# Kernel tuning notes

Hardware: AMD Instinct MI355X
Metric: run time of the kernel (lower is better)

## Reference

```python
import jax, jax.numpy as jnp
import numpy as np


def setup_inputs() -> dict:
    key = jax.random.key(0)
    ks = jax.random.split(key, 8)
    n_src, n_dst, n_edges = 100000, 50000, 600000
    d_in, d_out = 128, 128
    n_reuse, n_cache = 5000, 8000
    full_dst_len = n_dst + n_reuse

    feat_src = jax.random.normal(ks[0], (n_src, d_in), jnp.float32)
    src = jax.random.randint(ks[1], (n_edges,), 0, n_src)
    dst = jax.random.randint(ks[2], (n_edges,), 0, n_dst)
    # xavier-ish init for the two bias-free Linear layers (stored as [out, in] like torch)
    W_self = jax.random.normal(ks[3], (d_out, d_in), jnp.float32) / np.sqrt(d_in).astype(np.float32)
    W_neigh = jax.random.normal(ks[4], (d_out, d_in), jnp.float32) / np.sqrt(d_in).astype(np.float32)
    # reuse_indices must be unique positions within [0, full_dst_len)
    reuse_indices = jnp.sort(jax.random.permutation(ks[5], full_dst_len)[:n_reuse])
    reuse_embedding = jax.random.normal(ks[6], (n_reuse, d_out), jnp.float32)
    cache_indices = jax.random.randint(ks[7], (n_cache,), 0, full_dst_len)
    return dict(feat_src=feat_src, W_self=W_self, W_neigh=W_neigh,
                reuse_embedding=reuse_embedding, src=src, dst=dst,
                reuse_indices=reuse_indices, cache_indices=cache_indices,
                n_dst=n_dst)


def reference(feat_src, W_self, W_neigh, reuse_embedding, src, dst,
              reuse_indices, cache_indices, n_dst):
    # --- GraphSAGE 'mean' aggregation on a block graph ---
    feat_dst = feat_src[:n_dst]                         # [n_dst, D_in]
    msgs = feat_src[src]                                # [E, D_in] copy_src gather
    ssum = jax.ops.segment_sum(msgs, dst, num_segments=n_dst)          # [n_dst, D_in]
    deg = jax.ops.segment_sum(jnp.ones_like(msgs[:, 0]), dst, num_segments=n_dst)
    h_neigh = jnp.where(deg[:, None] > 0, ssum / jnp.maximum(deg, 1.0)[:, None], 0.0)
    rst = feat_dst @ W_self.T + h_neigh @ W_neigh.T     # fc_self + fc_neigh

    # --- cache-reuse scatter merge (flag == 0 path) ---
    n_reuse = reuse_indices.shape[0]
    full_dst_len = n_dst + n_reuse
    keep = jnp.ones((full_dst_len,), dtype=bool).at[reuse_indices].set(False)
    unprune_indices = jnp.nonzero(keep, size=n_dst)[0]  # np.delete equivalent
    full = jnp.zeros((full_dst_len, rst.shape[1]), rst.dtype)
    full = full.at[unprune_indices].set(rst).at[reuse_indices].set(reuse_embedding)
    cache_embedding = jax.lax.stop_gradient(full[cache_indices])  # .detach()
    return full, cache_embedding
```

## Files before the change

kernel.cpp:

```cpp
#include <hip/hip_runtime.h>

#define N_SRC   100000
#define N_DST   50000
#define D       128
#define MAXDEG  64

#define TOTAL_BLOCKS 2048
#define EDGE_BLOCKS  512

typedef __attribute__((ext_vector_type(8))) short bf16x8;
typedef __attribute__((ext_vector_type(4))) float f32x4;

__device__ __forceinline__ unsigned short f2bf(float f) {
    unsigned u = __float_as_uint(f);
    u += 0x7FFFu + ((u >> 16) & 1u);
    return (unsigned short)(u >> 16);
}
__device__ __forceinline__ float bf2f(unsigned short u) {
    return __uint_as_float((unsigned)u << 16);
}

__global__ __launch_bounds__(256)
void prep_build_kernel(const int* __restrict__ src,
                       const int* __restrict__ dst,
                       int* __restrict__ ell,
                       int* __restrict__ cnt,
                       int n_edges,
                       const int* __restrict__ reuse_idx,
                       int* __restrict__ rowpos, int n_reuse,
                       const float* __restrict__ Wself,
                       const float* __restrict__ Wneigh,
                       unsigned short* __restrict__ wbf,
                       const float* __restrict__ feat,
                       unsigned int* __restrict__ featbf_u32) {
    if (blockIdx.x < EDGE_BLOCKS) {
        int eid = blockIdx.x * 256 + threadIdx.x;
        const int estride = EDGE_BLOCKS * 256;
        for (int e0 = eid; e0 < n_edges; e0 += 4 * estride) {
            int e1 = e0 + estride, e2 = e0 + 2 * estride, e3 = e0 + 3 * estride;
            bool v1 = e1 < n_edges, v2 = e2 < n_edges, v3 = e3 < n_edges;
            int d0 = dst[e0], s0 = src[e0];
            int d1 = 0, s1 = 0, d2 = 0, s2 = 0, d3 = 0, s3 = 0;
            if (v1) { d1 = dst[e1]; s1 = src[e1]; }
            if (v2) { d2 = dst[e2]; s2 = src[e2]; }
            if (v3) { d3 = dst[e3]; s3 = src[e3]; }
            int p0 = atomicAdd(&cnt[d0], 1);
            int p1 = v1 ? atomicAdd(&cnt[d1], 1) : MAXDEG;
            int p2 = v2 ? atomicAdd(&cnt[d2], 1) : MAXDEG;
            int p3 = v3 ? atomicAdd(&cnt[d3], 1) : MAXDEG;
            if (p0 < MAXDEG) ell[(size_t)d0 * MAXDEG + p0] = s0;
            if (p1 < MAXDEG) ell[(size_t)d1 * MAXDEG + p1] = s1;
            if (p2 < MAXDEG) ell[(size_t)d2 * MAXDEG + p2] = s2;
            if (p3 < MAXDEG) ell[(size_t)d3 * MAXDEG + p3] = s3;
        }
    } else {
        int stid = (blockIdx.x - EDGE_BLOCKS) * 256 + threadIdx.x;
        const int sstride = (TOTAL_BLOCKS - EDGE_BLOCKS) * 256;

        if (stid < N_DST) {
            int lo = 0, hi = n_reuse;
            while (lo < hi) {
                int mid = (lo + hi) >> 1;
                if (reuse_idx[mid] - mid > stid) hi = mid; else lo = mid + 1;
            }
            rowpos[stid] = stid + lo;
        }

        if (stid < 128 * 256) {
            int n = stid >> 8;
            int k = stid & 255;
            float v = (k < 128) ? Wself[n * 128 + k] : Wneigh[n * 128 + (k - 128)];
            wbf[stid] = f2bf(v);
        }

        const int n4 = N_SRC * (D / 4);
        for (int i = stid; i < n4; i += sstride) {
            float4 v = *(const float4*)(feat + (size_t)i * 4);
            uint2 o;
            o.x = (unsigned)f2bf(v.x) | ((unsigned)f2bf(v.y) << 16);
            o.y = (unsigned)f2bf(v.z) | ((unsigned)f2bf(v.w) << 16);
            *(uint2*)(featbf_u32 + (size_t)i * 2) = o;
        }
    }
}

__global__ __launch_bounds__(256)
void gather_bf16_kernel(const unsigned short* __restrict__ featbf,
                        const int* __restrict__ ell,
                        const int* __restrict__ cnt,
                        uint4* __restrict__ hneigh_u4) {
    int gid  = blockIdx.x * blockDim.x + threadIdx.x;
    int row  = gid >> 4;
    int lane = gid & 15;
    if (row >= N_DST) return;

    int deg = cnt[row];
    int n = min(deg, MAXDEG);
    float inv = 1.0f / fmaxf((float)deg, 1.0f);
    const int* rell = ell + (size_t)row * MAXDEG;

    float acc[8];
#pragma unroll
    for (int k = 0; k < 8; ++k) acc[k] = 0.f;

    union U { uint4 v; unsigned short us[8]; };
    int j = 0;
    for (; j + 4 <= n; j += 4) {
        int s0 = rell[j + 0];
        int s1 = rell[j + 1];
        int s2 = rell[j + 2];
        int s3 = rell[j + 3];
        U a, b, c, d;
        a.v = *(const uint4*)(featbf + (size_t)s0 * D + lane * 8);
        b.v = *(const uint4*)(featbf + (size_t)s1 * D + lane * 8);
        c.v = *(const uint4*)(featbf + (size_t)s2 * D + lane * 8);
        d.v = *(const uint4*)(featbf + (size_t)s3 * D + lane * 8);
#pragma unroll
        for (int k = 0; k < 8; ++k)
            acc[k] += (bf2f(a.us[k]) + bf2f(b.us[k])) + (bf2f(c.us[k]) + bf2f(d.us[k]));
    }
    for (; j < n; ++j) {
        int s = rell[j];
        U a;
        a.v = *(const uint4*)(featbf + (size_t)s * D + lane * 8);
#pragma unroll
        for (int k = 0; k < 8; ++k) acc[k] += bf2f(a.us[k]);
    }
    uint4 o;
    o.x = (unsigned)f2bf(acc[0] * inv) | ((unsigned)f2bf(acc[1] * inv) << 16);
    o.y = (unsigned)f2bf(acc[2] * inv) | ((unsigned)f2bf(acc[3] * inv) << 16);
    o.z = (unsigned)f2bf(acc[4] * inv) | ((unsigned)f2bf(acc[5] * inv) << 16);
    o.w = (unsigned)f2bf(acc[6] * inv) | ((unsigned)f2bf(acc[7] * inv) << 16);
    hneigh_u4[(size_t)row * 16 + lane] = o;
}

__global__ __launch_bounds__(256, 2)
void gemm_kernel(const unsigned short* __restrict__ featbf,
                 const unsigned short* __restrict__ hneigh,
                 const unsigned short* __restrict__ wbf,
                 const int* __restrict__ rowpos,
                 float* __restrict__ full) {
    __shared__ unsigned short Wl[128 * 256];

    int tid = threadIdx.x;
    {
        int n = tid >> 1;
        int ckbase = (tid & 1) * 16;
        const uint4* s = (const uint4*)(wbf + n * 256);
        uint4* d = (uint4*)(Wl + n * 256);
#pragma unroll
        for (int i = 0; i < 16; ++i) {
            int ck = ckbase + i;
            d[ck ^ (n & 7)] = s[ck];
        }
    }
    __syncthreads();

    int wv   = tid >> 6;
    int lane = tid & 63;
    int l15  = lane & 15;
    int q    = lane >> 4;
    int rowbase = blockIdx.x * 128 + wv * 32;

    f32x4 acc[2][8];
#pragma unroll
    for (int rt = 0; rt < 2; ++rt)
#pragma unroll
        for (int ct = 0; ct < 8; ++ct) acc[rt][ct] = (f32x4){0.f, 0.f, 0.f, 0.f};

    int r0c = min(rowbase + l15,      N_DST - 1);
    int r1c = min(rowbase + 16 + l15, N_DST - 1);

#pragma unroll
    for (int s = 0; s < 8; ++s) {
        const unsigned short* A = (s < 4) ? featbf : hneigh;
        int k0 = (s & 3) * 32 + q * 8;
        bf16x8 a0 = *(const bf16x8*)(A + (size_t)r0c * D + k0);
        bf16x8 a1 = *(const bf16x8*)(A + (size_t)r1c * D + k0);
#pragma unroll
        for (int ct = 0; ct < 8; ++ct) {
            int n = ct * 16 + l15;
            int ck = s * 4 + q;
            bf16x8 b = *(const bf16x8*)(Wl + n * 256 + ((ck ^ (n & 7)) << 3));
            acc[0][ct] = __builtin_amdgcn_mfma_f32_16x16x32_bf16(a0, b, acc[0][ct], 0, 0, 0);
            acc[1][ct] = __builtin_amdgcn_mfma_f32_16x16x32_bf16(a1, b, acc[1][ct], 0, 0, 0);
        }
    }

#pragma unroll
    for (int rt = 0; rt < 2; ++rt) {
#pragma unroll
        for (int reg = 0; reg < 4; ++reg) {
            int gm = rowbase + rt * 16 + q * 4 + reg;
            if (gm < N_DST) {
                int jj = rowpos[gm];
                float* outr = full + (size_t)jj * D + l15;
#pragma unroll
                for (int ct = 0; ct < 8; ++ct)
                    outr[ct * 16] = acc[rt][ct][reg];
            }
        }
    }
}

__global__ __launch_bounds__(256)
void epilogue_kernel(const float* __restrict__ emb,
                     const int* __restrict__ ridx, int n_reuse,
                     float* __restrict__ full,
                     const int* __restrict__ cidx,
                     float* __restrict__ cache_out, int n_cache) {
    int idx = blockIdx.x * blockDim.x + threadIdx.x;
    int row = idx >> 5;
    int c4 = (idx & 31) * 4;
    if (row < n_reuse) {
        *(float4*)&full[(size_t)ridx[row] * D + c4] =
            *(const float4*)&emb[(size_t)row * D + c4];
    } else if (row < n_reuse + n_cache) {
        int r = row - n_reuse;
        int v = cidx[r];
        int lo = 0, hi = n_reuse;
        while (lo < hi) {
            int mid = (lo + hi) >> 1;
            if (ridx[mid] < v) lo = mid + 1; else hi = mid;
        }
        const float* srcp = (lo < n_reuse && ridx[lo] == v)
            ? emb + (size_t)lo * D
            : full + (size_t)v * D;
        *(float4*)&cache_out[(size_t)r * D + c4] = *(const float4*)&srcp[c4];
    }
}

extern "C" void kernel_launch(void* const* d_in, const int* in_sizes, int n_in,
                              void* d_out, int out_size, void* d_ws, size_t ws_size,
                              hipStream_t stream) {
    const float* feat_src  = (const float*)d_in[0];
    const float* W_self    = (const float*)d_in[1];
    const float* W_neigh   = (const float*)d_in[2];
    const float* reuse_emb = (const float*)d_in[3];
    const int*   src       = (const int*)d_in[4];
    const int*   dst       = (const int*)d_in[5];
    const int*   reuse_idx = (const int*)d_in[6];
    const int*   cache_idx = (const int*)d_in[7];

    int n_edges = in_sizes[4];
    int n_reuse = in_sizes[6];
    int n_cache = in_sizes[7];
    int full_len = N_DST + n_reuse;

    float* full = (float*)d_out;
    float* cache_out = full + (size_t)full_len * D;

    size_t hneigh_b = (size_t)N_DST * D * sizeof(unsigned short);
    size_t featbf_b = (size_t)N_SRC * D * sizeof(unsigned short);

    unsigned short* hneigh = (unsigned short*)d_ws;
    unsigned short* featbf = (unsigned short*)((char*)d_ws + hneigh_b);
    int*   cnt    = (int*)((char*)featbf + featbf_b);
    int*   rowpos = cnt + N_DST;
    unsigned short* wbf = (unsigned short*)(rowpos + N_DST);

    int* ell = (int*)full;

    hipMemsetAsync(cnt, 0, (size_t)N_DST * sizeof(int), stream);

    prep_build_kernel<<<TOTAL_BLOCKS, 256, 0, stream>>>(
        src, dst, ell, cnt, n_edges,
        reuse_idx, rowpos, n_reuse, W_self, W_neigh, wbf,
        feat_src, (unsigned int*)featbf);

    gather_bf16_kernel<<<(N_DST * 16 + 255) / 256, 256, 0, stream>>>(
        featbf, ell, cnt, (uint4*)hneigh);

    gemm_kernel<<<(N_DST + 127) / 128, 256, 0, stream>>>(
        featbf, hneigh, wbf, rowpos, full);

    epilogue_kernel<<<((n_reuse + n_cache) * 32 + 255) / 256, 256, 0, stream>>>(
        reuse_emb, reuse_idx, n_reuse, full, cache_idx, cache_out, n_cache);
}
```

Before: 196.7 us.

## Build ELL adjacency via two-level bucket counting sort instead of global atomics

Replaces the global-atomic ELL construction with a counting sort. Edges are first counted per coarse bucket of 128 destination rows in shared memory, then scanned, scattered into bucket-contiguous pairs, and finally placed into ELL slots using shared-memory atomics per bucket. This removes global atomic contention, scattered ELL writes and the count memset, but adds three extra kernel launches, a single-block serial scan, and an intermediate edge-pair buffer.

```diff
diff --git a/kernel.cpp b/kernel.cpp
--- a/kernel.cpp
+++ b/kernel.cpp
@@ -5,8 +5,10 @@
 #define D       128
 #define MAXDEG  64
 
+#define NB      391
+#define CHUNKS  256
 #define TOTAL_BLOCKS 2048
-#define EDGE_BLOCKS  512
+#define COUNT_BLOCKS 256
 
 typedef __attribute__((ext_vector_type(8))) short bf16x8;
 typedef __attribute__((ext_vector_type(4))) float f32x4;
@@ -21,11 +23,9 @@
 }
 
 __global__ __launch_bounds__(256)
-void prep_build_kernel(const int* __restrict__ src,
-                       const int* __restrict__ dst,
-                       int* __restrict__ ell,
-                       int* __restrict__ cnt,
-                       int n_edges,
+void prep_count_kernel(const int* __restrict__ dst,
+                       int* __restrict__ cntmat,
+                       int n_edges, int cb,
                        const int* __restrict__ reuse_idx,
                        int* __restrict__ rowpos, int n_reuse,
                        const float* __restrict__ Wself,
@@ -33,29 +33,20 @@
                        unsigned short* __restrict__ wbf,
                        const float* __restrict__ feat,
                        unsigned int* __restrict__ featbf_u32) {
-    if (blockIdx.x < EDGE_BLOCKS) {
-        int eid = blockIdx.x * 256 + threadIdx.x;
-        const int estride = EDGE_BLOCKS * 256;
-        for (int e0 = eid; e0 < n_edges; e0 += 4 * estride) {
-            int e1 = e0 + estride, e2 = e0 + 2 * estride, e3 = e0 + 3 * estride;
-            bool v1 = e1 < n_edges, v2 = e2 < n_edges, v3 = e3 < n_edges;
-            int d0 = dst[e0], s0 = src[e0];
-            int d1 = 0, s1 = 0, d2 = 0, s2 = 0, d3 = 0, s3 = 0;
-            if (v1) { d1 = dst[e1]; s1 = src[e1]; }
-            if (v2) { d2 = dst[e2]; s2 = src[e2]; }
-            if (v3) { d3 = dst[e3]; s3 = src[e3]; }
-            int p0 = atomicAdd(&cnt[d0], 1);
-            int p1 = v1 ? atomicAdd(&cnt[d1], 1) : MAXDEG;
-            int p2 = v2 ? atomicAdd(&cnt[d2], 1) : MAXDEG;
-            int p3 = v3 ? atomicAdd(&cnt[d3], 1) : MAXDEG;
-            if (p0 < MAXDEG) ell[(size_t)d0 * MAXDEG + p0] = s0;
-            if (p1 < MAXDEG) ell[(size_t)d1 * MAXDEG + p1] = s1;
-            if (p2 < MAXDEG) ell[(size_t)d2 * MAXDEG + p2] = s2;
-            if (p3 < MAXDEG) ell[(size_t)d3 * MAXDEG + p3] = s3;
-        }
+    __shared__ int lc[NB];
+    if (blockIdx.x < COUNT_BLOCKS) {
+        for (int i = threadIdx.x; i < NB; i += 256) lc[i] = 0;
+        __syncthreads();
+        int c = blockIdx.x;
+        int e0 = c * cb, e1 = min(n_edges, e0 + cb);
+        for (int e = e0 + (int)threadIdx.x; e < e1; e += 256)
+            atomicAdd(&lc[dst[e] >> 7], 1);
+        __syncthreads();
+        for (int i = threadIdx.x; i < NB; i += 256)
+            cntmat[c * NB + i] = lc[i];
     } else {
-        int stid = (blockIdx.x - EDGE_BLOCKS) * 256 + threadIdx.x;
-        const int sstride = (TOTAL_BLOCKS - EDGE_BLOCKS) * 256;
+        int stid = (blockIdx.x - COUNT_BLOCKS) * 256 + threadIdx.x;
+        const int sstride = (TOTAL_BLOCKS - COUNT_BLOCKS) * 256;
 
         if (stid < N_DST) {
             int lo = 0, hi = n_reuse;
@@ -65,14 +56,12 @@
             }
             rowpos[stid] = stid + lo;
         }
-
         if (stid < 128 * 256) {
             int n = stid >> 8;
             int k = stid & 255;
             float v = (k < 128) ? Wself[n * 128 + k] : Wneigh[n * 128 + (k - 128)];
             wbf[stid] = f2bf(v);
         }
-
         const int n4 = N_SRC * (D / 4);
         for (int i = stid; i < n4; i += sstride) {
             float4 v = *(const float4*)(feat + (size_t)i * 4);
@@ -82,6 +71,78 @@
             *(uint2*)(featbf_u32 + (size_t)i * 2) = o;
         }
     }
+}
+
+__global__ __launch_bounds__(256)
+void scan_kernel(const int* __restrict__ cntmat,
+                 int* __restrict__ offmat,
+                 int* __restrict__ bucketbase) {
+    __shared__ int bsum[NB];
+    __shared__ int bbase[NB + 1];
+    int t = threadIdx.x;
+    for (int k = t; k < NB; k += 256) {
+        int s = 0;
+        for (int c = 0; c < CHUNKS; ++c) s += cntmat[c * NB + k];
+        bsum[k] = s;
+    }
+    __syncthreads();
+    if (t == 0) {
+        int run = 0;
+        for (int k = 0; k < NB; ++k) { bbase[k] = run; run += bsum[k]; }
+        bbase[NB] = run;
+    }
+    __syncthreads();
+    for (int k = t; k < NB + 1; k += 256) bucketbase[k] = bbase[k];
+    for (int k = t; k < NB; k += 256) {
+        int run = bbase[k];
+        for (int c = 0; c < CHUNKS; ++c) {
+            offmat[k * CHUNKS + c] = run;
+            run += cntmat[c * NB + k];
+        }
+    }
+}
+
+__global__ __launch_bounds__(256)
+void scatter_kernel(const int* __restrict__ src,
+                    const int* __restrict__ dst,
+                    const int* __restrict__ offmat,
+                    uint2* __restrict__ pe,
+                    int n_edges, int cb) {
+    __shared__ int lc[NB];
+    for (int i = threadIdx.x; i < NB; i += 256) lc[i] = 0;
+    __syncthreads();
+    int c = blockIdx.x;
+    int e0 = c * cb, e1 = min(n_edges, e0 + cb);
+    for (int e = e0 + (int)threadIdx.x; e < e1; e += 256) {
+        int d = dst[e];
+        int s = src[e];
+        int k = d >> 7;
+        int r = atomicAdd(&lc[k], 1);
+        int pos = offmat[k * CHUNKS + c] + r;
+        pe[pos] = make_uint2((unsigned)s, (unsigned)d);
+    }
+}
+
+__global__ __launch_bounds__(256)
+void fine_ell_kernel(const uint2* __restrict__ pe,
+                     const int* __restrict__ bucketbase,
+                     int* __restrict__ ell,
+                     int* __restrict__ cnt) {
+    __shared__ int rc[128];
+    int k = blockIdx.x;
+    if (threadIdx.x < 128) rc[threadIdx.x] = 0;
+    __syncthreads();
+    int e0 = bucketbase[k], e1 = bucketbase[k + 1];
+    for (int e = e0 + (int)threadIdx.x; e < e1; e += 256) {
+        uint2 p = pe[e];
+        int d = (int)p.y;
+        int slot = atomicAdd(&rc[d & 127], 1);
+        if (slot < MAXDEG)
+            ell[(size_t)d * MAXDEG + slot] = (int)p.x;
+    }
+    __syncthreads();
+    int row = k * 128 + threadIdx.x;
+    if (threadIdx.x < 128 && row < N_DST) cnt[row] = rc[threadIdx.x];
 }
 
 __global__ __launch_bounds__(256)
@@ -246,6 +307,7 @@
     int n_reuse = in_sizes[6];
     int n_cache = in_sizes[7];
     int full_len = N_DST + n_reuse;
+    int cb = (n_edges + CHUNKS - 1) / CHUNKS;
 
     float* full = (float*)d_out;
     float* cache_out = full + (size_t)full_len * D;
@@ -258,16 +320,27 @@
     int*   cnt    = (int*)((char*)featbf + featbf_b);
     int*   rowpos = cnt + N_DST;
     unsigned short* wbf = (unsigned short*)(rowpos + N_DST);
+    int*   cntmat = (int*)(wbf + 128 * 256);
+    int*   offmat = cntmat + CHUNKS * NB;
+    int*   bucketbase = offmat + NB * CHUNKS;
+    uint2* pe = (uint2*)(bucketbase + NB + 2);
+
+    pe = (uint2*)(((size_t)pe + 7) & ~(size_t)7);
 
     int* ell = (int*)full;
 
-    hipMemsetAsync(cnt, 0, (size_t)N_DST * sizeof(int), stream);
-
-    prep_build_kernel<<<TOTAL_BLOCKS, 256, 0, stream>>>(
-        src, dst, ell, cnt, n_edges,
+    prep_count_kernel<<<TOTAL_BLOCKS, 256, 0, stream>>>(
+        dst, cntmat, n_edges, cb,
         reuse_idx, rowpos, n_reuse, W_self, W_neigh, wbf,
         feat_src, (unsigned int*)featbf);
 
+    scan_kernel<<<1, 256, 0, stream>>>(cntmat, offmat, bucketbase);
+
+    scatter_kernel<<<CHUNKS, 256, 0, stream>>>(
+        src, dst, offmat, pe, n_edges, cb);
+
+    fine_ell_kernel<<<NB, 256, 0, stream>>>(pe, bucketbase, ell, cnt);
+
     gather_bf16_kernel<<<(N_DST * 16 + 255) / 256, 256, 0, stream>>>(
         featbf, ell, cnt, (uint4*)hneigh);
 
```

New measurement: 218.3 us. 11.0% more time.
